# Kernel optimization log

Hardware: AMD Instinct MI355X
Metric: run time of the kernel (lower is better)

The kernel has to match this reference:

```python
import jax, jax.numpy as jnp
import numpy as np

B, L = 4, 40960
C = 512
DMLP = 2048
TEMP = 1e-5
EPS = 1e-5
FACTOR = 2  # Smartpool factor at layer 4


def setup_inputs() -> dict:
    key = jax.random.key(0)
    ks = jax.random.split(key, 8)

    def w(k, shape, fan_in):
        return jax.random.normal(k, shape, jnp.float32) / np.float32(np.sqrt(fan_in))

    inp = {
        "x": jax.random.normal(ks[0], (B, 1, L), jnp.float32),
        "conv0_w": w(ks[1], (C, 1, 10), 10),   "conv0_b": jnp.zeros(C, jnp.float32),
        "conv1_w": w(ks[2], (C, C, 8), C * 8), "conv1_b": jnp.zeros(C, jnp.float32),
        "conv2_w": w(ks[3], (C, C, 4), C * 4), "conv2_b": jnp.zeros(C, jnp.float32),
        "conv3_w": w(ks[4], (C, C, 4), C * 4), "conv3_b": jnp.zeros(C, jnp.float32),
        "mlp_w1": w(ks[5], (C, DMLP), C),       "mlp_b1": jnp.zeros(DMLP, jnp.float32),
        "mlp_w2": w(ks[6], (DMLP, DMLP), DMLP), "mlp_b2": jnp.zeros(DMLP, jnp.float32),
        "mlp_w3": w(ks[7], (DMLP, 1), DMLP),    "mlp_b3": jnp.zeros(1, jnp.float32),
    }
    for i in range(5):  # ChannelNorm affine params (init: ones/zeros)
        inp[f"n{i}_w"] = jnp.ones(C, jnp.float32)
        inp[f"n{i}_b"] = jnp.zeros(C, jnp.float32)
    return inp


def _conv(x, w, b, stride, pad):
    # Conv1d with padding_mode='reflect': reflect-pad then VALID conv. x: [B,C,T]
    x = jnp.pad(x, ((0, 0), (0, 0), (pad, pad)), mode="reflect")
    y = jax.lax.conv_general_dilated(x, w, (stride,), "VALID",
                                     dimension_numbers=("NCH", "OIH", "NCH"))
    return y + b[None, :, None]


def _cnorm(x, g, b):
    # ChannelNorm: normalize over channel dim with unbiased variance (torch.var default)
    m = jnp.mean(x, axis=1, keepdims=True)
    v = jnp.var(x, axis=1, keepdims=True, ddof=1)
    return (x - m) * jax.lax.rsqrt(v + EPS) * g[None, :, None] + b[None, :, None]


def _forward(x, conv0_w, conv0_b, conv1_w, conv1_b, conv2_w, conv2_b, conv3_w, conv3_b,
             n0_w, n0_b, n1_w, n1_b, n2_w, n2_b, n3_w, n3_b, n4_w, n4_b,
             mlp_w1, mlp_b1, mlp_w2, mlp_b2, mlp_w3, mlp_b3):
    h = jax.nn.relu(_cnorm(_conv(x, conv0_w, conv0_b, 5, 3), n0_w, n0_b))
    h = jax.nn.relu(_cnorm(_conv(h, conv1_w, conv1_b, 4, 2), n1_w, n1_b))
    h = jax.nn.relu(_cnorm(_conv(h, conv2_w, conv2_b, 2, 1), n2_w, n2_b))
    h = jax.nn.relu(_cnorm(_conv(h, conv3_w, conv3_b, 2, 1), n3_w, n3_b))

    f = jnp.transpose(h, (0, 2, 1))  # [B,T,C]
    T = f.shape[1]

    # importance MLP (dropout inactive in eval), exact GELU, sigmoid head
    z = jax.nn.gelu(f @ mlp_w1 + mlp_b1, approximate=False)
    z = jax.nn.gelu(z @ mlp_w2 + mlp_b2, approximate=False)
    imp = jax.nn.sigmoid((z @ mlp_w3 + mlp_b3)[..., 0]) + TEMP          # [B,T]
    imp = imp / jnp.sum(imp, axis=1, keepdims=True) * (T / FACTOR)      # sums to T/factor

    # warp: cumsum -> ramp contributions -> 2x2 [[-1,1],[1,-1]] conv = double diff
    Tn = T // FACTOR  # == round(importance_cs[0,-1])
    cs = jnp.cumsum(imp, axis=1)                                        # [B,T]
    p = jnp.maximum(cs[:, :, None] - jnp.arange(Tn, dtype=cs.dtype)[None, None, :], 0.0)  # [B,T,Tn]
    pc = jnp.pad(p, ((0, 0), (0, 0), (0, 1)))
    d = pc[:, :, :-1] - pc[:, :, 1:]                                    # diff along new-time axis
    wmat = d - jnp.pad(d, ((0, 0), (1, 0), (0, 0)))[:, :-1, :]          # diff along old-time axis, [B,T,Tn]
    pooled = jnp.einsum("btn,btc->bnc", wmat, f)                        # interp_weights @ X

    out = jnp.transpose(pooled, (0, 2, 1))                              # [B,C,Tn]
    return jax.nn.relu(_cnorm(out, n4_w, n4_b))


def reference(x, conv0_w, conv0_b, conv1_w, conv1_b, conv2_w, conv2_b, conv3_w, conv3_b,
              n0_w, n0_b, n1_w, n1_b, n2_w, n2_b, n3_w, n3_b, n4_w, n4_b,
              mlp_w1, mlp_b1, mlp_w2, mlp_b2, mlp_w3, mlp_b3):
    return _forward(x, conv0_w, conv0_b, conv1_w, conv1_b, conv2_w, conv2_b, conv3_w, conv3_b,
                    n0_w, n0_b, n1_w, n1_b, n2_w, n2_b, n3_w, n3_b, n4_w, n4_b,
                    mlp_w1, mlp_b1, mlp_w2, mlp_b2, mlp_w3, mlp_b3)
```

## Files before the change

kernel.cpp:

```cpp
#include <hip/hip_runtime.h>
#include <hip/hip_bf16.h>
#include <math.h>

#define NB 4
#define LIN 40960
#define NC 512
#define T0 8192
#define T1 2048
#define T2 1024
#define T3 512
#define TN 256
#define DM 2048
#define EPSF 1e-5f
#define TEMPF 1e-5f

typedef __attribute__((ext_vector_type(8))) short bf16x8;
typedef __attribute__((ext_vector_type(4))) float f32x4;

__device__ __forceinline__ int refl(int t, int T) {
  if (t < 0) t = -t;
  if (t >= T) t = 2 * T - 2 - t;
  return t;
}

__device__ __forceinline__ void gld16(void* lds, const void* g) {
  __builtin_amdgcn_global_load_lds((const __attribute__((address_space(1))) unsigned int*)g,
                                   (__attribute__((address_space(3))) unsigned int*)lds, 16, 0, 0);
}

__device__ __forceinline__ void blk_sum2_512(float& a, float& b, float* scratch) {
#pragma unroll
  for (int off = 32; off > 0; off >>= 1) {
    a += __shfl_down(a, off, 64);
    b += __shfl_down(b, off, 64);
  }
  int lane = threadIdx.x & 63, wid = threadIdx.x >> 6;
  __syncthreads();
  if (lane == 0) { scratch[wid] = a; scratch[8 + wid] = b; }
  __syncthreads();
  float sa = 0.f, sb = 0.f;
#pragma unroll
  for (int i = 0; i < 8; i++) { sa += scratch[i]; sb += scratch[8 + i]; }
  a = sa; b = sb;
}

template <int KT>
__device__ __forceinline__ void prep_conv_body(const float* __restrict__ w, __hip_bfloat16* __restrict__ wt,
                                               int co, float* l) {
  const float* wb = w + (size_t)co * 512 * KT;
  for (int i = threadIdx.x; i < 512 * KT; i += 256) l[i] = wb[i];
  __syncthreads();
  __hip_bfloat16* wo = wt + (size_t)co * 512 * KT;
  for (int i = threadIdx.x; i < 512 * KT; i += 256) {
    int kk = i >> 9, ci = i & 511;
    wo[i] = __float2bfloat16(l[ci * KT + kk]);
  }
}

template <int KD, int ND>
__device__ __forceinline__ void prep_mlp_body(const float* __restrict__ w, __hip_bfloat16* __restrict__ wt,
                                              int bidx, float* sbuf) {
  float(*tile)[33] = (float(*)[33])sbuf;
  int bx = bidx % (ND / 32);
  int by = bidx / (ND / 32);
  int tx = threadIdx.x & 31, ty = threadIdx.x >> 5;
#pragma unroll
  for (int i = 0; i < 32; i += 8)
    tile[ty + i][tx] = w[(size_t)(by * 32 + ty + i) * ND + bx * 32 + tx];
  __syncthreads();
#pragma unroll
  for (int i = 0; i < 32; i += 8)
    wt[(size_t)(bx * 32 + ty + i) * KD + by * 32 + tx] = __float2bfloat16(tile[tx][ty + i]);
}

__global__ __launch_bounds__(256) void k_prepA(const float* c1w, const float* c2w, const float* c3w,
                                               const float* mw1, __hip_bfloat16* wt1, __hip_bfloat16* wt2,
                                               __hip_bfloat16* wt3, __hip_bfloat16* wm1t) {
  __shared__ float sb[4096];
  int b = blockIdx.x;
  if (b < 512) prep_conv_body<8>(c1w, wt1, b, sb);
  else if (b < 1024) prep_conv_body<4>(c2w, wt2, b - 512, sb);
  else if (b < 1536) prep_conv_body<4>(c3w, wt3, b - 1024, sb);
  else prep_mlp_body<512, 2048>(mw1, wm1t, b - 1536, sb);
}

__global__ __launch_bounds__(256) void k_prepB(const float* mw2, __hip_bfloat16* wm2t) {
  __shared__ float sb[1056];
  prep_mlp_body<2048, 2048>(mw2, wm2t, blockIdx.x, sb);
}

__global__ __launch_bounds__(512) void k_conv0(const float* __restrict__ x, const float* __restrict__ w,
                                               const float* __restrict__ bias, const float* __restrict__ gw,
                                               const float* __restrict__ gb, __hip_bfloat16* __restrict__ out) {
  __shared__ float xv[48];
  __shared__ float tb[512 * 9];
  __shared__ float stats[16];
  int b = blockIdx.x / (T0 / 8);
  int t0 = (blockIdx.x % (T0 / 8)) * 8;
  int tid = threadIdx.x;
  if (tid < 45) xv[tid] = x[(size_t)b * LIN + refl(t0 * 5 - 3 + tid, LIN)];
  __syncthreads();
  float wk[10];
#pragma unroll
  for (int k = 0; k < 10; k++) wk[k] = w[tid * 10 + k];
  float bs = bias[tid];
  float acc[8];
#pragma unroll
  for (int tt = 0; tt < 8; tt++) {
    float a = bs;
#pragma unroll
    for (int k = 0; k < 10; k++) a += xv[tt * 5 + k] * wk[k];
    acc[tt] = a;
    tb[tid * 9 + tt] = a;
  }
  __syncthreads();
  int wave = tid >> 6, lane = tid & 63;
  float s = 0.f, q = 0.f;
#pragma unroll
  for (int j = 0; j < 8; j++) {
    float v = tb[(lane * 8 + j) * 9 + wave];
    s += v; q += v * v;
  }
#pragma unroll
  for (int off = 32; off > 0; off >>= 1) {
    s += __shfl_xor(s, off, 64);
    q += __shfl_xor(q, off, 64);
  }
  if (lane == 0) {
    float mean = s * (1.f / NC);
    float var = fmaxf((q - s * s * (1.f / NC)) * (1.f / (NC - 1)), 0.f);
    stats[wave] = mean;
    stats[8 + wave] = rsqrtf(var + EPSF);
  }
  __syncthreads();
  float gwv = gw[tid], gbv = gb[tid];
#pragma unroll
  for (int tt = 0; tt < 8; tt++) {
    float y = (acc[tt] - stats[tt]) * stats[8 + tt] * gwv + gbv;
    out[((size_t)(b * T0 + t0 + tt)) * NC + tid] = __float2bfloat16(fmaxf(y, 0.f));
  }
}

template <int MODE, int TIN_, int TOUT_, int SS, int PP, int KK, int NN, int SPLITK, int MM>
__global__ __launch_bounds__(256) void k_gemm2(const __hip_bfloat16* __restrict__ A,
                                               const __hip_bfloat16* __restrict__ Bt,
                                               float* __restrict__ Cf) {
  __shared__ __align__(16) __hip_bfloat16 sA[2][128 * 32];
  __shared__ __align__(16) __hip_bfloat16 sB[2][128 * 32];
  const int tid = threadIdx.x;
  const int lane = tid & 63;
  const int wave = tid >> 6;
  const int wm = wave >> 1, wn = wave & 1;
  constexpr int nt = NN / 128;
  constexpr int PS = (MM / 1024) * nt;
  constexpr int KBT = KK / 32;
  const int blk = blockIdx.x;
  const int xs = blk & 7, sl = blk >> 3;
  const int sk = sl / PS, rem = sl % PS;
  const int row0 = ((rem / nt) * 8 + xs) * 128;
  const int col0 = (rem % nt) * 128;
  const int kb0 = (sk * KBT) / SPLITK, kb1 = ((sk + 1) * KBT) / SPLITK;
  const int cq = lane >> 4, cl = lane & 15;

  auto stage = [&](int kb, int buf) {
#pragma unroll
    for (int rr = 0; rr < 2; rr++) {
      int c = rr * 256 + tid;
      int m = c >> 2, kc = c & 3;
      int kcs = kc ^ (m & 3);
      size_t ga;
      if (MODE == 0) {
        ga = (size_t)(row0 + m) * KK + kb * 32 + kcs * 8;
      } else {
        int r = row0 + m;
        int bb = r / TOUT_;
        int t = r - bb * TOUT_;
        int k = (kb * 32) >> 9;
        int ci = ((kb * 32) & 511) + kcs * 8;
        int gt = refl(t * SS - PP + k, TIN_);
        ga = (((size_t)(bb * TIN_ + gt)) << 9) + ci;
      }
      gld16((char*)&sA[buf][0] + c * 16, (const char*)(A + ga));
    }
#pragma unroll
    for (int rr = 0; rr < 2; rr++) {
      int c = rr * 256 + tid;
      int n = c >> 2, kc = c & 3;
      int kcs = kc ^ (n & 3);
      gld16((char*)&sB[buf][0] + c * 16, (const char*)(Bt + (size_t)(col0 + n) * KK + kb * 32 + kcs * 8));
    }
  };

  f32x4 acc[4][4];
  const f32x4 zz = {0.f, 0.f, 0.f, 0.f};
#pragma unroll
  for (int mi = 0; mi < 4; mi++)
#pragma unroll
    for (int ni = 0; ni < 4; ni++) acc[mi][ni] = zz;

  stage(kb0, 0);
  const int p = cq ^ (cl & 3);
  for (int kb = kb0; kb < kb1; kb++) {
    int cur = (kb - kb0) & 1;
    __syncthreads();
    if (kb + 1 < kb1) stage(kb + 1, cur ^ 1);
    const short* bA = (const short*)&sA[cur][0];
    const short* bB = (const short*)&sB[cur][0];
    bf16x8 af[4], bfr[4];
#pragma unroll
    for (int mi = 0; mi < 4; mi++)
      af[mi] = *(const bf16x8*)(bA + (wm * 64 + mi * 16 + cl) * 32 + p * 8);
#pragma unroll
    for (int ni = 0; ni < 4; ni++)
      bfr[ni] = *(const bf16x8*)(bB + (wn * 64 + ni * 16 + cl) * 32 + p * 8);
#pragma unroll
    for (int mi = 0; mi < 4; mi++)
#pragma unroll
      for (int ni = 0; ni < 4; ni++)
        acc[mi][ni] = __builtin_amdgcn_mfma_f32_16x16x32_bf16(af[mi], bfr[ni], acc[mi][ni], 0, 0, 0);
  }

#pragma unroll
  for (int mi = 0; mi < 4; mi++)
#pragma unroll
    for (int ni = 0; ni < 4; ni++)
#pragma unroll
      for (int r2 = 0; r2 < 4; r2++) {
        int row = row0 + wm * 64 + mi * 16 + cq * 4 + r2;
        int col = col0 + wn * 64 + ni * 16 + cl;
        Cf[(size_t)sk * MM * NN + (size_t)row * NN + col] = acc[mi][ni][r2];
      }
}

template <int MODE, int TIN_, int TOUT_, int SS, int PP, int KK, int NN, int EPI, int SPLITK, int MM>
__global__ __launch_bounds__(256) void k_gemm(const __hip_bfloat16* __restrict__ A,
                                              const __hip_bfloat16* __restrict__ Bt,
                                              const float* __restrict__ bias,
                                              float* __restrict__ Cf,
                                              __hip_bfloat16* __restrict__ Cb) {
  __shared__ __align__(16) __hip_bfloat16 sA[2][64 * 32];
  __shared__ __align__(16) __hip_bfloat16 sB[2][128 * 32];
  const int tid = threadIdx.x;
  const int lane = tid & 63;
  const int wave = tid >> 6;
  const int wm = wave >> 1, wn = wave & 1;
  constexpr int nt = NN / 128;
  constexpr int PS = (MM / 512) * nt;
  constexpr int KBT = KK / 32;
  const int blk = blockIdx.x;
  const int xs = blk & 7, sl = blk >> 3;
  const int sk = sl / PS, rem = sl % PS;
  const int row0 = ((rem / nt) * 8 + xs) * 64;
  const int col0 = (rem % nt) * 128;
  const int kb0 = (sk * KBT) / SPLITK, kb1 = ((sk + 1) * KBT) / SPLITK;
  const int cq = lane >> 4, cl = lane & 15;

  auto stage = [&](int kb, int buf) {
    {
      int m = tid >> 2, kc = tid & 3;
      int kcs = kc ^ (m & 3);
      size_t ga;
      if (MODE == 0) {
        ga = (size_t)(row0 + m) * KK + kb * 32 + kcs * 8;
      } else {
        int r = row0 + m;
        int bb = r / TOUT_;
        int t = r - bb * TOUT_;
        int k = (kb * 32) >> 9;
        int ci = ((kb * 32) & 511) + kcs * 8;
        int gt = refl(t * SS - PP + k, TIN_);
        ga = (((size_t)(bb * TIN_ + gt)) << 9) + ci;
      }
      gld16((char*)&sA[buf][0] + tid * 16, (const char*)(A + ga));
    }
#pragma unroll
    for (int rr = 0; rr < 2; rr++) {
      int c = rr * 256 + tid;
      int n = c >> 2, kc = c & 3;
      int kcs = kc ^ (n & 3);
      gld16((char*)&sB[buf][0] + c * 16, (const char*)(Bt + (size_t)(col0 + n) * KK + kb * 32 + kcs * 8));
    }
  };

  f32x4 acc[2][4];
  const f32x4 zz = {0.f, 0.f, 0.f, 0.f};
#pragma unroll
  for (int mi = 0; mi < 2; mi++)
#pragma unroll
    for (int ni = 0; ni < 4; ni++) acc[mi][ni] = zz;

  stage(kb0, 0);
  const int p = cq ^ (cl & 3);
  for (int kb = kb0; kb < kb1; kb++) {
    int cur = (kb - kb0) & 1;
    __syncthreads();
    if (kb + 1 < kb1) stage(kb + 1, cur ^ 1);
    const short* bA = (const short*)&sA[cur][0];
    const short* bB = (const short*)&sB[cur][0];
    bf16x8 af[2], bfr[4];
#pragma unroll
    for (int mi = 0; mi < 2; mi++)
      af[mi] = *(const bf16x8*)(bA + (wm * 32 + mi * 16 + cl) * 32 + p * 8);
#pragma unroll
    for (int ni = 0; ni < 4; ni++)
      bfr[ni] = *(const bf16x8*)(bB + (wn * 64 + ni * 16 + cl) * 32 + p * 8);
#pragma unroll
    for (int mi = 0; mi < 2; mi++)
#pragma unroll
      for (int ni = 0; ni < 4; ni++)
        acc[mi][ni] = __builtin_amdgcn_mfma_f32_16x16x32_bf16(af[mi], bfr[ni], acc[mi][ni], 0, 0, 0);
  }

#pragma unroll
  for (int mi = 0; mi < 2; mi++)
#pragma unroll
    for (int ni = 0; ni < 4; ni++)
#pragma unroll
      for (int r2 = 0; r2 < 4; r2++) {
        int row = row0 + wm * 32 + mi * 16 + cq * 4 + r2;
        int col = col0 + wn * 64 + ni * 16 + cl;
        float v = acc[mi][ni][r2];
        if (EPI == 1) {
          v += bias[col];
          v = 0.5f * v * (1.f + erff(v * 0.70710678118654752f));
          Cb[(size_t)row * NN + col] = __float2bfloat16(v);
        } else {
          Cf[(size_t)sk * MM * NN + (size_t)row * NN + col] = v;
        }
      }
}

template <int NS>
__global__ __launch_bounds__(512) void k_cnorm(const float* __restrict__ g, const float* __restrict__ cb,
                                               const float* __restrict__ gw, const float* __restrict__ gb,
                                               __hip_bfloat16* __restrict__ out, size_t stride) {
  int wave = threadIdx.x >> 6, lane = threadIdx.x & 63;
  size_t row = (size_t)blockIdx.x * 8 + wave;
  float v[8];
  {
    float4 c0 = *(const float4*)(cb + lane * 8), c1 = *(const float4*)(cb + lane * 8 + 4);
    v[0] = c0.x; v[1] = c0.y; v[2] = c0.z; v[3] = c0.w;
    v[4] = c1.x; v[5] = c1.y; v[6] = c1.z; v[7] = c1.w;
  }
#pragma unroll
  for (int s = 0; s < NS; s++) {
    const float* gr = g + s * stride + row * NC + lane * 8;
    float4 a0 = *(const float4*)gr;
    float4 a1 = *(const float4*)(gr + 4);
    v[0] += a0.x; v[1] += a0.y; v[2] += a0.z; v[3] += a0.w;
    v[4] += a1.x; v[5] += a1.y; v[6] += a1.z; v[7] += a1.w;
  }
  float s = 0.f, q = 0.f;
#pragma unroll
  for (int j = 0; j < 8; j++) { s += v[j]; q += v[j] * v[j]; }
#pragma unroll
  for (int off = 32; off > 0; off >>= 1) {
    s += __shfl_xor(s, off, 64);
    q += __shfl_xor(q, off, 64);
  }
  float mean = s * (1.f / NC);
  float var = fmaxf((q - s * s * (1.f / NC)) * (1.f / (NC - 1)), 0.f);
  float rstd = rsqrtf(var + EPSF);
  float4 w0 = *(const float4*)(gw + lane * 8), w1 = *(const float4*)(gw + lane * 8 + 4);
  float4 b0 = *(const float4*)(gb + lane * 8), b1 = *(const float4*)(gb + lane * 8 + 4);
  float gwv[8] = {w0.x, w0.y, w0.z, w0.w, w1.x, w1.y, w1.z, w1.w};
  float gbv[8] = {b0.x, b0.y, b0.z, b0.w, b1.x, b1.y, b1.z, b1.w};
  union { __hip_bfloat16 h[8]; uint4 u; } pk;
#pragma unroll
  for (int j = 0; j < 8; j++)
    pk.h[j] = __float2bfloat16(fmaxf((v[j] - mean) * rstd * gwv[j] + gbv[j], 0.f));
  *(uint4*)(out + row * NC + lane * 8) = pk.u;
}

template <int NS>
__global__ __launch_bounds__(256) void k_head(const float* __restrict__ g, const float* __restrict__ b2,
                                              const float* __restrict__ w3, const float* __restrict__ b3,
                                              float* __restrict__ imp) {
  __shared__ float red[4];
  int row = blockIdx.x, tid = threadIdx.x;
  int c = tid * 8;
  float v[8];
  {
    float4 x0 = *(const float4*)(b2 + c), x1 = *(const float4*)(b2 + c + 4);
    v[0] = x0.x; v[1] = x0.y; v[2] = x0.z; v[3] = x0.w;
    v[4] = x1.x; v[5] = x1.y; v[6] = x1.z; v[7] = x1.w;
  }
#pragma unroll
  for (int s = 0; s < NS; s++) {
    const float* gr = g + (size_t)s * (2048 * DM) + (size_t)row * DM + c;
    float4 a0 = *(const float4*)gr;
    float4 a1 = *(const float4*)(gr + 4);
    v[0] += a0.x; v[1] += a0.y; v[2] += a0.z; v[3] += a0.w;
    v[4] += a1.x; v[5] += a1.y; v[6] += a1.z; v[7] += a1.w;
  }
  float a = 0.f;
  float4 w0 = *(const float4*)(w3 + c), w1 = *(const float4*)(w3 + c + 4);
  float wv[8] = {w0.x, w0.y, w0.z, w0.w, w1.x, w1.y, w1.z, w1.w};
#pragma unroll
  for (int j = 0; j < 8; j++) {
    float z = 0.5f * v[j] * (1.f + erff(v[j] * 0.70710678118654752f));
    a += z * wv[j];
  }
#pragma unroll
  for (int off = 32; off > 0; off >>= 1) a += __shfl_down(a, off, 64);
  int lane = tid & 63, wid = tid >> 6;
  if (lane == 0) red[wid] = a;
  __syncthreads();
  if (tid == 0) {
    float s = red[0] + red[1] + red[2] + red[3] + b3[0];
    imp[row] = 1.f / (1.f + expf(-s)) + TEMPF;
  }
}

__device__ __forceinline__ float dfun(float cv, int n) {
  float d = fmaxf(cv - (float)n, 0.f);
  if (n < TN - 1) d = fminf(d, 1.f);
  return d;
}

__global__ __launch_bounds__(512) void k_poolfinal(const __hip_bfloat16* __restrict__ f,
                                                   const float* __restrict__ imp,
                                                   const float* __restrict__ gw, const float* __restrict__ gb,
                                                   float* __restrict__ out) {
  __shared__ float wt[T3];
  __shared__ float wsum[8];
  __shared__ float red[16];
  int b = blockIdx.x / TN, n = blockIdx.x % TN;
  int tid = threadIdx.x, wave = tid >> 6, lane = tid & 63;
  float own = imp[b * T3 + tid];
  float s = own;
#pragma unroll
  for (int off = 1; off < 64; off <<= 1) {
    float t = __shfl_up(s, off, 64);
    if (lane >= off) s += t;
  }
  if (lane == 63) wsum[wave] = s;
  __syncthreads();
  float prefix = 0.f, total = 0.f;
#pragma unroll
  for (int w = 0; w < 8; w++) {
    float ws_ = wsum[w];
    total += ws_;
    if (w < wave) prefix += ws_;
  }
  float scale = (float)TN / total;
  float incl = (prefix + s) * scale;
  float excl = (prefix + s - own) * scale;
  wt[tid] = dfun(incl, n) - dfun(excl, n);
  __syncthreads();
  float acc = 0.f;
  for (int t = 0; t < T3; t++) {
    float w = wt[t];
    if (w != 0.f) acc += w * __bfloat162float(f[((size_t)b * T3 + t) * NC + tid]);
  }
  float sv = acc, q = acc * acc;
  blk_sum2_512(sv, q, red);
  float mean = sv * (1.f / NC);
  float var = fmaxf((q - sv * sv * (1.f / NC)) * (1.f / (NC - 1)), 0.f);
  float y = (acc - mean) * rsqrtf(var + EPSF) * gw[tid] + gb[tid];
  out[((size_t)b * NC + tid) * TN + n] = fmaxf(y, 0.f);
}

extern "C" void kernel_launch(void* const* d_in, const int* in_sizes, int n_in,
                              void* d_out, int out_size, void* d_ws, size_t ws_size,
                              hipStream_t stream) {
  const float* x   = (const float*)d_in[0];
  const float* c0w = (const float*)d_in[1];  const float* c0b = (const float*)d_in[2];
  const float* c1w = (const float*)d_in[3];  const float* c1b = (const float*)d_in[4];
  const float* c2w = (const float*)d_in[5];  const float* c2b = (const float*)d_in[6];
  const float* c3w = (const float*)d_in[7];  const float* c3b = (const float*)d_in[8];
  const float* mw1 = (const float*)d_in[9];  const float* mb1 = (const float*)d_in[10];
  const float* mw2 = (const float*)d_in[11]; const float* mb2 = (const float*)d_in[12];
  const float* mw3 = (const float*)d_in[13]; const float* mb3 = (const float*)d_in[14];
  const float* n0w = (const float*)d_in[15]; const float* n0b = (const float*)d_in[16];
  const float* n1w = (const float*)d_in[17]; const float* n1b = (const float*)d_in[18];
  const float* n2w = (const float*)d_in[19]; const float* n2b = (const float*)d_in[20];
  const float* n3w = (const float*)d_in[21]; const float* n3b = (const float*)d_in[22];
  const float* n4w = (const float*)d_in[23]; const float* n4b = (const float*)d_in[24];

  char* base = (char*)d_ws;
  __hip_bfloat16* h0b  = (__hip_bfloat16*)(base);
  __hip_bfloat16* h1b  = (__hip_bfloat16*)(base);
  __hip_bfloat16* h2b  = (__hip_bfloat16*)(base + (8u << 20));
  __hip_bfloat16* h3b  = (__hip_bfloat16*)(base + (12u << 20));
  __hip_bfloat16* z1b  = (__hip_bfloat16*)(base + (14u << 20));
  float*          imp  = (float*)(base + (22u << 20));
  float*          g    = (float*)(base + (32u << 20));
  __hip_bfloat16* wm1t = (__hip_bfloat16*)(base + (80u << 20));
  __hip_bfloat16* wt2  = (__hip_bfloat16*)(base + (82u << 20));
  __hip_bfloat16* wt3  = (__hip_bfloat16*)(base + (84u << 20));
  __hip_bfloat16* wt1  = (__hip_bfloat16*)(base + (86u << 20));
  __hip_bfloat16* wm2t = (__hip_bfloat16*)(base + (86u << 20));
  float* outp = (float*)d_out;

  k_prepA<<<2560, 256, 0, stream>>>(c1w, c2w, c3w, mw1, wt1, wt2, wt3, wm1t);
  k_conv0<<<NB * (T0 / 8), 512, 0, stream>>>(x, c0w, c0b, n0w, n0b, h0b);

  k_gemm2<1, 8192, 2048, 4, 2, 4096, 512, 3, 8192><<<768, 256, 0, stream>>>(h0b, wt1, g);
  k_prepB<<<4096, 256, 0, stream>>>(mw2, wm2t);
  k_cnorm<3><<<8192 / 8, 512, 0, stream>>>(g, c1b, n1w, n1b, h1b, (size_t)8192 * 512);
  k_gemm2<1, 2048, 1024, 2, 1, 2048, 512, 6, 4096><<<768, 256, 0, stream>>>(h1b, wt2, g);
  k_cnorm<6><<<4096 / 8, 512, 0, stream>>>(g, c2b, n2w, n2b, h2b, (size_t)4096 * 512);
  k_gemm<1, 1024, 512, 2, 1, 2048, 512, 0, 6, 2048><<<768, 256, 0, stream>>>(h2b, wt3, nullptr, g, nullptr);
  k_cnorm<6><<<2048 / 8, 512, 0, stream>>>(g, c3b, n3w, n3b, h3b, (size_t)2048 * 512);

  k_gemm<0, 0, 1, 0, 0, 512, 2048, 1, 1, 2048><<<512, 256, 0, stream>>>(h3b, wm1t, mb1, nullptr, z1b);
  k_gemm2<0, 0, 1, 0, 0, 2048, 2048, 3, 2048><<<768, 256, 0, stream>>>(z1b, wm2t, g);

  k_head<3><<<NB * T3, 256, 0, stream>>>(g, mb2, mw3, mb3, imp);
  k_poolfinal<<<NB * TN, 512, 0, stream>>>(h3b, imp, n4w, n4b, outp);
}
```

Measured before the change: 343.8 us.

## Store split-K partials in bf16, raise split counts, merge weight prep kernels

Split-K GEMM partial sums are now written as bf16 rather than fp32, and the channel-norm and head reduction kernels read them as bf16. This halves partial-sum traffic. The split-K factors are raised (3→4, 6→8) so each GEMM launches 1024 blocks for better occupancy. The two weight-prep kernels are merged into one launch, and the workspace layout is reshuffled. Rounding each partial to bf16 before the reduction adds error and could affect accuracy.

```diff
diff --git a/kernel.cpp b/kernel.cpp
--- a/kernel.cpp
+++ b/kernel.cpp
@@ -44,6 +44,13 @@
   a = sa; b = sb;
 }
 
+__device__ __forceinline__ void add_bf8(const __hip_bfloat16* p, float* v) {
+  union { uint4 u; __hip_bfloat16 h[8]; } pk;
+  pk.u = *(const uint4*)p;
+#pragma unroll
+  for (int j = 0; j < 8; j++) v[j] += __bfloat162float(pk.h[j]);
+}
+
 template <int KT>
 __device__ __forceinline__ void prep_conv_body(const float* __restrict__ w, __hip_bfloat16* __restrict__ wt,
                                                int co, float* l) {
@@ -73,20 +80,18 @@
     wt[(size_t)(bx * 32 + ty + i) * KD + by * 32 + tx] = __float2bfloat16(tile[tx][ty + i]);
 }
 
-__global__ __launch_bounds__(256) void k_prepA(const float* c1w, const float* c2w, const float* c3w,
-                                               const float* mw1, __hip_bfloat16* wt1, __hip_bfloat16* wt2,
-                                               __hip_bfloat16* wt3, __hip_bfloat16* wm1t) {
+__global__ __launch_bounds__(256) void k_prep(const float* c1w, const float* c2w, const float* c3w,
+                                              const float* mw1, const float* mw2,
+                                              __hip_bfloat16* wt1, __hip_bfloat16* wt2,
+                                              __hip_bfloat16* wt3, __hip_bfloat16* wm1t,
+                                              __hip_bfloat16* wm2t) {
   __shared__ float sb[4096];
   int b = blockIdx.x;
   if (b < 512) prep_conv_body<8>(c1w, wt1, b, sb);
   else if (b < 1024) prep_conv_body<4>(c2w, wt2, b - 512, sb);
   else if (b < 1536) prep_conv_body<4>(c3w, wt3, b - 1024, sb);
-  else prep_mlp_body<512, 2048>(mw1, wm1t, b - 1536, sb);
-}
-
-__global__ __launch_bounds__(256) void k_prepB(const float* mw2, __hip_bfloat16* wm2t) {
-  __shared__ float sb[1056];
-  prep_mlp_body<2048, 2048>(mw2, wm2t, blockIdx.x, sb);
+  else if (b < 2560) prep_mlp_body<512, 2048>(mw1, wm1t, b - 1536, sb);
+  else prep_mlp_body<2048, 2048>(mw2, wm2t, b - 2560, sb);
 }
 
 __global__ __launch_bounds__(512) void k_conv0(const float* __restrict__ x, const float* __restrict__ w,
@@ -144,7 +149,7 @@
 template <int MODE, int TIN_, int TOUT_, int SS, int PP, int KK, int NN, int SPLITK, int MM>
 __global__ __launch_bounds__(256) void k_gemm2(const __hip_bfloat16* __restrict__ A,
                                                const __hip_bfloat16* __restrict__ Bt,
-                                               float* __restrict__ Cf) {
+                                               __hip_bfloat16* __restrict__ Cp) {
   __shared__ __align__(16) __hip_bfloat16 sA[2][128 * 32];
   __shared__ __align__(16) __hip_bfloat16 sB[2][128 * 32];
   const int tid = threadIdx.x;
@@ -228,7 +233,7 @@
       for (int r2 = 0; r2 < 4; r2++) {
         int row = row0 + wm * 64 + mi * 16 + cq * 4 + r2;
         int col = col0 + wn * 64 + ni * 16 + cl;
-        Cf[(size_t)sk * MM * NN + (size_t)row * NN + col] = acc[mi][ni][r2];
+        Cp[(size_t)sk * MM * NN + (size_t)row * NN + col] = __float2bfloat16(acc[mi][ni][r2]);
       }
 }
 
@@ -236,8 +241,7 @@
 __global__ __launch_bounds__(256) void k_gemm(const __hip_bfloat16* __restrict__ A,
                                               const __hip_bfloat16* __restrict__ Bt,
                                               const float* __restrict__ bias,
-                                              float* __restrict__ Cf,
-                                              __hip_bfloat16* __restrict__ Cb) {
+                                              __hip_bfloat16* __restrict__ Cout) {
   __shared__ __align__(16) __hip_bfloat16 sA[2][64 * 32];
   __shared__ __align__(16) __hip_bfloat16 sB[2][128 * 32];
   const int tid = threadIdx.x;
@@ -323,15 +327,16 @@
         if (EPI == 1) {
           v += bias[col];
           v = 0.5f * v * (1.f + erff(v * 0.70710678118654752f));
-          Cb[(size_t)row * NN + col] = __float2bfloat16(v);
+          Cout[(size_t)row * NN + col] = __float2bfloat16(v);
         } else {
-          Cf[(size_t)sk * MM * NN + (size_t)row * NN + col] = v;
+          Cout[(size_t)sk * MM * NN + (size_t)row * NN + col] = __float2bfloat16(v);
         }
       }
 }
 
 template <int NS>
-__global__ __launch_bounds__(512) void k_cnorm(const float* __restrict__ g, const float* __restrict__ cb,
+__global__ __launch_bounds__(512) void k_cnorm(const __hip_bfloat16* __restrict__ g,
+                                               const float* __restrict__ cb,
                                                const float* __restrict__ gw, const float* __restrict__ gb,
                                                __hip_bfloat16* __restrict__ out, size_t stride) {
   int wave = threadIdx.x >> 6, lane = threadIdx.x & 63;
@@ -343,13 +348,7 @@
     v[4] = c1.x; v[5] = c1.y; v[6] = c1.z; v[7] = c1.w;
   }
 #pragma unroll
-  for (int s = 0; s < NS; s++) {
-    const float* gr = g + s * stride + row * NC + lane * 8;
-    float4 a0 = *(const float4*)gr;
-    float4 a1 = *(const float4*)(gr + 4);
-    v[0] += a0.x; v[1] += a0.y; v[2] += a0.z; v[3] += a0.w;
-    v[4] += a1.x; v[5] += a1.y; v[6] += a1.z; v[7] += a1.w;
-  }
+  for (int s = 0; s < NS; s++) add_bf8(g + s * stride + row * NC + lane * 8, v);
   float s = 0.f, q = 0.f;
 #pragma unroll
   for (int j = 0; j < 8; j++) { s += v[j]; q += v[j] * v[j]; }
@@ -373,7 +372,8 @@
 }
 
 template <int NS>
-__global__ __launch_bounds__(256) void k_head(const float* __restrict__ g, const float* __restrict__ b2,
+__global__ __launch_bounds__(256) void k_head(const __hip_bfloat16* __restrict__ g,
+                                              const float* __restrict__ b2,
                                               const float* __restrict__ w3, const float* __restrict__ b3,
                                               float* __restrict__ imp) {
   __shared__ float red[4];
@@ -386,13 +386,7 @@
     v[4] = x1.x; v[5] = x1.y; v[6] = x1.z; v[7] = x1.w;
   }
 #pragma unroll
-  for (int s = 0; s < NS; s++) {
-    const float* gr = g + (size_t)s * (2048 * DM) + (size_t)row * DM + c;
-    float4 a0 = *(const float4*)gr;
-    float4 a1 = *(const float4*)(gr + 4);
-    v[0] += a0.x; v[1] += a0.y; v[2] += a0.z; v[3] += a0.w;
-    v[4] += a1.x; v[5] += a1.y; v[6] += a1.z; v[7] += a1.w;
-  }
+  for (int s = 0; s < NS; s++) add_bf8(g + (size_t)s * (2048 * DM) + (size_t)row * DM + c, v);
   float a = 0.f;
   float4 w0 = *(const float4*)(w3 + c), w1 = *(const float4*)(w3 + c + 4);
   float wv[8] = {w0.x, w0.y, w0.z, w0.w, w1.x, w1.y, w1.z, w1.w};
@@ -485,28 +479,27 @@
   __hip_bfloat16* h3b  = (__hip_bfloat16*)(base + (12u << 20));
   __hip_bfloat16* z1b  = (__hip_bfloat16*)(base + (14u << 20));
   float*          imp  = (float*)(base + (22u << 20));
-  float*          g    = (float*)(base + (32u << 20));
-  __hip_bfloat16* wm1t = (__hip_bfloat16*)(base + (80u << 20));
-  __hip_bfloat16* wt2  = (__hip_bfloat16*)(base + (82u << 20));
-  __hip_bfloat16* wt3  = (__hip_bfloat16*)(base + (84u << 20));
-  __hip_bfloat16* wt1  = (__hip_bfloat16*)(base + (86u << 20));
-  __hip_bfloat16* wm2t = (__hip_bfloat16*)(base + (86u << 20));
+  __hip_bfloat16* g    = (__hip_bfloat16*)(base + (32u << 20));
+  __hip_bfloat16* wm1t = (__hip_bfloat16*)(base + (64u << 20));
+  __hip_bfloat16* wt2  = (__hip_bfloat16*)(base + (66u << 20));
+  __hip_bfloat16* wt3  = (__hip_bfloat16*)(base + (68u << 20));
+  __hip_bfloat16* wt1  = (__hip_bfloat16*)(base + (70u << 20));
+  __hip_bfloat16* wm2t = (__hip_bfloat16*)(base + (74u << 20));
   float* outp = (float*)d_out;
 
-  k_prepA<<<2560, 256, 0, stream>>>(c1w, c2w, c3w, mw1, wt1, wt2, wt3, wm1t);
+  k_prep<<<6656, 256, 0, stream>>>(c1w, c2w, c3w, mw1, mw2, wt1, wt2, wt3, wm1t, wm2t);
   k_conv0<<<NB * (T0 / 8), 512, 0, stream>>>(x, c0w, c0b, n0w, n0b, h0b);
 
-  k_gemm2<1, 8192, 2048, 4, 2, 4096, 512, 3, 8192><<<768, 256, 0, stream>>>(h0b, wt1, g);
-  k_prepB<<<4096, 256, 0, stream>>>(mw2, wm2t);
-  k_cnorm<3><<<8192 / 8, 512, 0, stream>>>(g, c1b, n1w, n1b, h1b, (size_t)8192 * 512);
-  k_gemm2<1, 2048, 1024, 2, 1, 2048, 512, 6, 4096><<<768, 256, 0, stream>>>(h1b, wt2, g);
-  k_cnorm<6><<<4096 / 8, 512, 0, stream>>>(g, c2b, n2w, n2b, h2b, (size_t)4096 * 512);
-  k_gemm<1, 1024, 512, 2, 1, 2048, 512, 0, 6, 2048><<<768, 256, 0, stream>>>(h2b, wt3, nullptr, g, nullptr);
-  k_cnorm<6><<<2048 / 8, 512, 0, stream>>>(g, c3b, n3w, n3b, h3b, (size_t)2048 * 512);
-
-  k_gemm<0, 0, 1, 0, 0, 512, 2048, 1, 1, 2048><<<512, 256, 0, stream>>>(h3b, wm1t, mb1, nullptr, z1b);
-  k_gemm2<0, 0, 1, 0, 0, 2048, 2048, 3, 2048><<<768, 256, 0, stream>>>(z1b, wm2t, g);
-
-  k_head<3><<<NB * T3, 256, 0, stream>>>(g, mb2, mw3, mb3, imp);
+  k_gemm2<1, 8192, 2048, 4, 2, 4096, 512, 4, 8192><<<1024, 256, 0, stream>>>(h0b, wt1, g);
+  k_cnorm<4><<<8192 / 8, 512, 0, stream>>>(g, c1b, n1w, n1b, h1b, (size_t)8192 * 512);
+  k_gemm2<1, 2048, 1024, 2, 1, 2048, 512, 8, 4096><<<1024, 256, 0, stream>>>(h1b, wt2, g);
+  k_cnorm<8><<<4096 / 8, 512, 0, stream>>>(g, c2b, n2w, n2b, h2b, (size_t)4096 * 512);
+  k_gemm<1, 1024, 512, 2, 1, 2048, 512, 0, 8, 2048><<<1024, 256, 0, stream>>>(h2b, wt3, nullptr, g);
+  k_cnorm<8><<<2048 / 8, 512, 0, stream>>>(g, c3b, n3w, n3b, h3b, (size_t)2048 * 512);
+
+  k_gemm<0, 0, 1, 0, 0, 512, 2048, 1, 1, 2048><<<512, 256, 0, stream>>>(h3b, wm1t, mb1, z1b);
+  k_gemm2<0, 0, 1, 0, 0, 2048, 2048, 4, 2048><<<1024, 256, 0, stream>>>(z1b, wm2t, g);
+
+  k_head<4><<<NB * T3, 256, 0, stream>>>(g, mb2, mw3, mb3, imp);
   k_poolfinal<<<NB * TN, 512, 0, stream>>>(h3b, imp, n4w, n4b, outp);
 }
```

Result: no change. 341.5 us (-0.7%).
